# Optimization experiments

Hardware: AMD Instinct MI355X
Metric: run time of the kernel (lower is better)

The kernel has to match this reference:

```python
import jax, jax.numpy as jnp
import numpy as np

B, S, HID = 2, 2048, 2048
H, KV, D = 8, 1, 256
BASE = 10000.0


def setup_inputs() -> dict:
    key = jax.random.key(0)
    ks = jax.random.split(key, 6)
    hidden_states = jax.random.normal(ks[0], (B, S, HID), dtype=jnp.float32)
    attention_mask = jnp.zeros((B, 1, S, S), dtype=jnp.float32)
    position_ids = jnp.sort(jax.random.randint(ks[1], (B, S), 0, S), axis=-1).astype(jnp.int64)
    sc = 1.0 / np.sqrt(HID)
    wq = jax.random.normal(ks[2], (H * D, HID), dtype=jnp.float32) * sc
    wk = jax.random.normal(ks[3], (KV * D, HID), dtype=jnp.float32) * sc
    wv = jax.random.normal(ks[4], (KV * D, HID), dtype=jnp.float32) * sc
    wo = jax.random.normal(ks[5], (HID, H * D), dtype=jnp.float32) * sc
    return {"hidden_states": hidden_states, "attention_mask": attention_mask,
            "position_ids": position_ids, "wq": wq, "wk": wk, "wv": wv, "wo": wo}


def _rotate_half(x):
    x1, x2 = jnp.split(x, 2, axis=-1)
    return jnp.concatenate((-x2, x1), axis=-1)


def reference(hidden_states, attention_mask, position_ids, wq, wk, wv, wo):
    b, s, _ = hidden_states.shape
    # QKV projections (no bias)
    q = (hidden_states @ wq.T).reshape(b, s, H, D).transpose(0, 2, 1, 3)   # [B,H,S,D]
    k = (hidden_states @ wk.T).reshape(b, s, KV, D).transpose(0, 2, 1, 3)  # [B,KV,S,D]
    v = (hidden_states @ wv.T).reshape(b, s, KV, D).transpose(0, 2, 1, 3)
    # RoPE: freqs = pos * inv_freq, emb = cat(freqs, freqs)
    inv_freq = 1.0 / (BASE ** (jnp.arange(0, D, 2, dtype=jnp.float32) / D))  # [D/2]
    freqs = position_ids.astype(jnp.float32)[:, :, None] * inv_freq[None, None, :]  # [B,S,D/2]
    emb = jnp.concatenate((freqs, freqs), axis=-1)                         # [B,S,D]
    cos = jnp.cos(emb)[:, None, :, :].astype(hidden_states.dtype)          # [B,1,S,D]
    sin = jnp.sin(emb)[:, None, :, :].astype(hidden_states.dtype)
    q = q * cos + _rotate_half(q) * sin
    k = k * cos + _rotate_half(k) * sin
    # repeat_kv: kv head outer, rep inner -> jnp.repeat along head axis
    n_rep = H // KV
    k = jnp.repeat(k, n_rep, axis=1)  # [B,H,S,D]
    v = jnp.repeat(v, n_rep, axis=1)
    scores = jnp.einsum('bhqd,bhkd->bhqk', q, k) / jnp.sqrt(jnp.float32(D))
    scores = scores + attention_mask
    attn = jax.nn.softmax(scores.astype(jnp.float32), axis=-1).astype(q.dtype)
    out = jnp.einsum('bhqk,bhkd->bhqd', attn, v)          # [B,H,S,D]
    out = out.transpose(0, 2, 1, 3).reshape(b, s, H * D)  # [B,S,H*D]
    return out @ wo.T
```

## Files before the change

### kernel.cpp

```cpp
#include <hip/hip_runtime.h>
#include <math.h>

#define B_ 2
#define S_ 2048
#define HID_ 2048
#define H_ 8
#define D_ 256
#define KV_STRIDE 512

typedef __attribute__((ext_vector_type(8))) __bf16 bf16x8;
typedef __attribute__((ext_vector_type(8))) unsigned short u16x8;
typedef __attribute__((ext_vector_type(4))) float f32x4;

__device__ __forceinline__ unsigned short bf16_rne(float x) {
    unsigned int u = __float_as_uint(x);
    return (unsigned short)((u + 0x7FFFu + ((u >> 16) & 1u)) >> 16);
}

__global__ __launch_bounds__(256) void split_bf16(const float* __restrict__ x,
                                                  unsigned short* __restrict__ h,
                                                  unsigned short* __restrict__ l,
                                                  int n4) {
    int i = blockIdx.x * 256 + threadIdx.x;
    if (i >= n4) return;
    float4 v = ((const float4*)x)[i];
    ushort4 hh, ll;
    hh.x = bf16_rne(v.x); ll.x = bf16_rne(v.x - __uint_as_float((unsigned int)hh.x << 16));
    hh.y = bf16_rne(v.y); ll.y = bf16_rne(v.y - __uint_as_float((unsigned int)hh.y << 16));
    hh.z = bf16_rne(v.z); ll.z = bf16_rne(v.z - __uint_as_float((unsigned int)hh.z << 16));
    hh.w = bf16_rne(v.w); ll.w = bf16_rne(v.w - __uint_as_float((unsigned int)hh.w << 16));
    ((ushort4*)h)[i] = hh;
    ((ushort4*)l)[i] = ll;
}

__global__ __launch_bounds__(256) void gemm_mfma_split(
    const unsigned short* __restrict__ Ah, const unsigned short* __restrict__ Al,
    const unsigned short* __restrict__ Wh, const unsigned short* __restrict__ Wl,
    float* __restrict__ C, int M, int N, int K)
{
    __shared__ unsigned short As[2][128][40];
    __shared__ unsigned short Bs[2][128][40];

    const int tid  = threadIdx.x;
    const int lane = tid & 63;
    const int w    = tid >> 6;
    const int wr   = w >> 1, wc = w & 1;
    const int fr   = lane & 15;
    const int ko   = (lane >> 4) * 8;
    const int bm   = blockIdx.x * 128, bn = blockIdx.y * 128;

    const int srow = tid >> 1;
    const int skc  = (tid & 1) * 16;
    const unsigned short* gAh = Ah + (size_t)(bm + srow) * K + skc;
    const unsigned short* gAl = Al + (size_t)(bm + srow) * K + skc;
    const unsigned short* gWh = Wh + (size_t)(bn + srow) * K + skc;
    const unsigned short* gWl = Wl + (size_t)(bn + srow) * K + skc;

    f32x4 acc[4][4];
#pragma unroll
    for (int i = 0; i < 4; ++i)
#pragma unroll
        for (int j = 0; j < 4; ++j)
#pragma unroll
            for (int r = 0; r < 4; ++r) acc[i][j][r] = 0.f;

    u16x8 ra0 = ((const u16x8*)gAh)[0], ra1 = ((const u16x8*)gAh)[1];
    u16x8 ra2 = ((const u16x8*)gAl)[0], ra3 = ((const u16x8*)gAl)[1];
    u16x8 rb0 = ((const u16x8*)gWh)[0], rb1 = ((const u16x8*)gWh)[1];
    u16x8 rb2 = ((const u16x8*)gWl)[0], rb3 = ((const u16x8*)gWl)[1];

    for (int k0 = 0; k0 < K; k0 += 32) {
        *(u16x8*)&As[0][srow][skc]     = ra0;
        *(u16x8*)&As[0][srow][skc + 8] = ra1;
        *(u16x8*)&As[1][srow][skc]     = ra2;
        *(u16x8*)&As[1][srow][skc + 8] = ra3;
        *(u16x8*)&Bs[0][srow][skc]     = rb0;
        *(u16x8*)&Bs[0][srow][skc + 8] = rb1;
        *(u16x8*)&Bs[1][srow][skc]     = rb2;
        *(u16x8*)&Bs[1][srow][skc + 8] = rb3;
        __syncthreads();

        if (k0 + 32 < K) {
            const unsigned short* nAh = gAh + k0 + 32;
            const unsigned short* nAl = gAl + k0 + 32;
            const unsigned short* nWh = gWh + k0 + 32;
            const unsigned short* nWl = gWl + k0 + 32;
            ra0 = ((const u16x8*)nAh)[0]; ra1 = ((const u16x8*)nAh)[1];
            ra2 = ((const u16x8*)nAl)[0]; ra3 = ((const u16x8*)nAl)[1];
            rb0 = ((const u16x8*)nWh)[0]; rb1 = ((const u16x8*)nWh)[1];
            rb2 = ((const u16x8*)nWl)[0]; rb3 = ((const u16x8*)nWl)[1];
        }

        bf16x8 ah[4], al4[4], bh[4], bl[4];
#pragma unroll
        for (int i = 0; i < 4; ++i) {
            ah[i]  = *(const bf16x8*)&As[0][wr * 64 + i * 16 + fr][ko];
            al4[i] = *(const bf16x8*)&As[1][wr * 64 + i * 16 + fr][ko];
            bh[i]  = *(const bf16x8*)&Bs[0][wc * 64 + i * 16 + fr][ko];
            bl[i]  = *(const bf16x8*)&Bs[1][wc * 64 + i * 16 + fr][ko];
        }
#pragma unroll
        for (int i = 0; i < 4; ++i)
#pragma unroll
            for (int j = 0; j < 4; ++j) {
                acc[i][j] = __builtin_amdgcn_mfma_f32_16x16x32_bf16(ah[i],  bh[j], acc[i][j], 0, 0, 0);
                acc[i][j] = __builtin_amdgcn_mfma_f32_16x16x32_bf16(ah[i],  bl[j], acc[i][j], 0, 0, 0);
                acc[i][j] = __builtin_amdgcn_mfma_f32_16x16x32_bf16(al4[i], bh[j], acc[i][j], 0, 0, 0);
            }
        __syncthreads();
    }

#pragma unroll
    for (int i = 0; i < 4; ++i) {
        int r0 = bm + wr * 64 + i * 16 + (lane >> 4) * 4;
#pragma unroll
        for (int j = 0; j < 4; ++j) {
            int c = bn + wc * 64 + j * 16 + fr;
#pragma unroll
            for (int r = 0; r < 4; ++r)
                C[(size_t)(r0 + r) * N + c] = acc[i][j][r];
        }
    }
}

__global__ __launch_bounds__(128) void rope_kernel(float* __restrict__ q,
                                                   const float* __restrict__ kv,
                                                   unsigned short* __restrict__ k_h,
                                                   unsigned short* __restrict__ k_l,
                                                   const int* __restrict__ pos) {
    int bs = blockIdx.x;
    int d = threadIdx.x;
    float p = (float)pos[bs];
    float inv = expf(-(2.0f * (float)d / (float)D_) * 9.210340371976184f);
    float sn, cs;
    sincosf(p * inv, &sn, &cs);

    float* qp = q + (size_t)bs * (H_ * D_);
#pragma unroll
    for (int h = 0; h < H_; ++h) {
        float x1 = qp[h * D_ + d];
        float x2 = qp[h * D_ + d + 128];
        qp[h * D_ + d]       = x1 * cs - x2 * sn;
        qp[h * D_ + d + 128] = x2 * cs + x1 * sn;
    }
    const float* kp = kv + (size_t)bs * KV_STRIDE;
    float x1 = kp[d], x2 = kp[d + 128];
    float y1 = x1 * cs - x2 * sn;
    float y2 = x2 * cs + x1 * sn;
    unsigned short h1 = bf16_rne(y1);
    unsigned short h2 = bf16_rne(y2);
    size_t o = (size_t)bs * D_ + d;
    k_h[o]       = h1;
    k_l[o]       = bf16_rne(y1 - __uint_as_float((unsigned int)h1 << 16));
    k_h[o + 128] = h2;
    k_l[o + 128] = bf16_rne(y2 - __uint_as_float((unsigned int)h2 << 16));
}

__global__ __launch_bounds__(256) void vsplitT(const float* __restrict__ kvb,
                                               unsigned short* __restrict__ vTh,
                                               unsigned short* __restrict__ vTl) {
    __shared__ float ts[64][65];
    const int blk = blockIdx.x;
    const int b  = blk >> 7;
    const int dt = (blk >> 5) & 3;
    const int jt = blk & 31;
    const int tid = threadIdx.x;
    const int jj = tid >> 2;
    const int dc = (tid & 3) * 16;
    const float* src = kvb + (size_t)(b * S_ + jt * 64 + jj) * KV_STRIDE + 256 + dt * 64 + dc;
#pragma unroll
    for (int i = 0; i < 16; i += 4) {
        float4 v4 = *(const float4*)(src + i);
        ts[jj][dc + i + 0] = v4.x;
        ts[jj][dc + i + 1] = v4.y;
        ts[jj][dc + i + 2] = v4.z;
        ts[jj][dc + i + 3] = v4.w;
    }
    __syncthreads();
    const int dd = tid >> 2;
    const int jc = (tid & 3) * 16;
    size_t o = (size_t)(b * 256 + dt * 64 + dd) * S_ + jt * 64 + jc;
#pragma unroll
    for (int i = 0; i < 16; i += 8) {
        u16x8 hh, ll;
#pragma unroll
        for (int e = 0; e < 8; ++e) {
            float f = ts[jc + i + e][dd];
            unsigned short hb = bf16_rne(f);
            hh[e] = hb;
            ll[e] = bf16_rne(f - __uint_as_float((unsigned int)hb << 16));
        }
        *(u16x8*)(vTh + o + i) = hh;
        *(u16x8*)(vTl + o + i) = ll;
    }
}

__global__ __launch_bounds__(512) void attn_mfma(
    const float* __restrict__ q,
    const unsigned short* __restrict__ k_h,
    const unsigned short* __restrict__ k_l,
    const unsigned short* __restrict__ vTh,
    const unsigned short* __restrict__ vTl,
    const float* __restrict__ mask,
    float* __restrict__ out)
{
    __shared__ __align__(16) unsigned short Ks[2][16][264];
    __shared__ __align__(16) unsigned short Vs[2][257][24];
    __shared__ __align__(16) unsigned short Ps[2][8][16][40];

    const int tid  = threadIdx.x;
    const int lane = tid & 63;
    const int w    = tid >> 6;
    const int fr   = lane & 15;
    const int kg   = lane >> 4;
    const int nqt  = S_ / 128;
    const int b    = blockIdx.x / (H_ * nqt);
    const int rem  = blockIdx.x % (H_ * nqt);
    const int h    = rem / nqt;
    const int i0   = (rem % nqt) * 128;

    {
        u16x8 z = {0, 0, 0, 0, 0, 0, 0, 0};
        unsigned short* vz = &Vs[0][0][0];
        for (int i = tid * 8; i < 12336; i += 512 * 8)
            *(u16x8*)(vz + i) = z;
        int pp = tid >> 8, pw = (tid >> 5) & 7, pr = (tid >> 1) & 15, ph8 = (tid & 1) * 8;
        *(u16x8*)&Ps[pp][pw][pr][16 + ph8] = z;
    }

    bf16x8 qh[8], ql[8];
    {
        const int qrow = i0 + w * 16 + fr;
        const float* qp = q + (size_t)(b * S_ + qrow) * (H_ * D_) + h * D_ + kg * 8;
#pragma unroll
        for (int ks = 0; ks < 8; ++ks) {
            float4 f0 = *(const float4*)(qp + ks * 32);
            float4 f1 = *(const float4*)(qp + ks * 32 + 4);
            float f[8] = {f0.x, f0.y, f0.z, f0.w, f1.x, f1.y, f1.z, f1.w};
            u16x8 hh, ll;
#pragma unroll
            for (int e = 0; e < 8; ++e) {
                unsigned short hb = bf16_rne(f[e]);
                hh[e] = hb;
                ll[e] = bf16_rne(f[e] - __uint_as_float((unsigned int)hb << 16));
            }
            qh[ks] = *(bf16x8*)&hh;
            ql[ks] = *(bf16x8*)&ll;
        }
    }

    f32x4 acc[16];
#pragma unroll
    for (int cf = 0; cf < 16; ++cf) acc[cf] = f32x4{0.f, 0.f, 0.f, 0.f};
    float m_run[4], l_run[4];
#pragma unroll
    for (int r = 0; r < 4; ++r) { m_run[r] = -1e30f; l_run[r] = 0.f; }

    const int skp = tid >> 8;
    const int skr = (tid >> 4) & 15;
    const int skc = (tid & 15) * 16;
    const int svd = tid & 255;
    const unsigned short* gK = (skp ? k_l : k_h) + (size_t)(b * S_ + skr) * 256 + skc;
    const unsigned short* gV = (skp ? vTl : vTh) + (size_t)(b * 256 + svd) * S_;

    u16x8 rk0 = *(const u16x8*)(gK);
    u16x8 rk1 = *(const u16x8*)(gK + 8);
    u16x8 rv0 = *(const u16x8*)(gV);
    u16x8 rv1 = *(const u16x8*)(gV + 8);

    const float scale = 0.0625f;

    for (int j0 = 0; j0 < S_; j0 += 16) {
        __syncthreads();
        *(u16x8*)&Ks[skp][skr][skc]     = rk0;
        *(u16x8*)&Ks[skp][skr][skc + 8] = rk1;
        *(u16x8*)&Vs[skp][svd][0]       = rv0;
        *(u16x8*)&Vs[skp][svd][8]       = rv1;
        if (j0 + 16 < S_) {
            rk0 = *(const u16x8*)(gK + (size_t)(j0 + 16) * 256);
            rk1 = *(const u16x8*)(gK + (size_t)(j0 + 16) * 256 + 8);
            rv0 = *(const u16x8*)(gV + j0 + 16);
            rv1 = *(const u16x8*)(gV + j0 + 24);
        }
        __syncthreads();

        f32x4 sc = {0.f, 0.f, 0.f, 0.f};
#pragma unroll
        for (int ks = 0; ks < 8; ++ks) {
            bf16x8 bh = *(const bf16x8*)&Ks[0][fr][ks * 32 + kg * 8];
            bf16x8 bl = *(const bf16x8*)&Ks[1][fr][ks * 32 + kg * 8];
            sc = __builtin_amdgcn_mfma_f32_16x16x32_bf16(qh[ks], bh, sc, 0, 0, 0);
            sc = __builtin_amdgcn_mfma_f32_16x16x32_bf16(qh[ks], bl, sc, 0, 0, 0);
            sc = __builtin_amdgcn_mfma_f32_16x16x32_bf16(ql[ks], bh, sc, 0, 0, 0);
        }

        float sv[4];
#pragma unroll
        for (int r = 0; r < 4; ++r)
            sv[r] = sc[r] * scale
                  + mask[(size_t)(b * S_ + i0 + w * 16 + kg * 4 + r) * S_ + j0 + fr];

        float rmax[4];
#pragma unroll
        for (int r = 0; r < 4; ++r) rmax[r] = sv[r];
#pragma unroll
        for (int off = 1; off < 16; off <<= 1)
#pragma unroll
            for (int r = 0; r < 4; ++r)
                rmax[r] = fmaxf(rmax[r], __shfl_xor(rmax[r], off));

        float corr[4], psum[4];
#pragma unroll
        for (int r = 0; r < 4; ++r) {
            float mn = fmaxf(m_run[r], rmax[r]);
            corr[r] = __expf(m_run[r] - mn);
            m_run[r] = mn;
            float p = __expf(sv[r] - mn);
            psum[r] = p;
            unsigned short phh = bf16_rne(p);
            Ps[0][w][kg * 4 + r][fr] = phh;
            Ps[1][w][kg * 4 + r][fr] = bf16_rne(p - __uint_as_float((unsigned int)phh << 16));
        }
#pragma unroll
        for (int off = 1; off < 16; off <<= 1)
#pragma unroll
            for (int r = 0; r < 4; ++r) psum[r] += __shfl_xor(psum[r], off);
#pragma unroll
        for (int r = 0; r < 4; ++r) l_run[r] = l_run[r] * corr[r] + psum[r];

#pragma unroll
        for (int cf = 0; cf < 16; ++cf)
#pragma unroll
            for (int r = 0; r < 4; ++r) acc[cf][r] *= corr[r];

        bf16x8 pah = *(const bf16x8*)&Ps[0][w][fr][kg * 8];
        bf16x8 pal = *(const bf16x8*)&Ps[1][w][fr][kg * 8];
#pragma unroll
        for (int cf = 0; cf < 16; ++cf) {
            bf16x8 vh = *(const bf16x8*)&Vs[0][cf * 16 + fr][kg * 8];
            bf16x8 vl = *(const bf16x8*)&Vs[1][cf * 16 + fr][kg * 8];
            acc[cf] = __builtin_amdgcn_mfma_f32_16x16x32_bf16(pah, vh, acc[cf], 0, 0, 0);
            acc[cf] = __builtin_amdgcn_mfma_f32_16x16x32_bf16(pah, vl, acc[cf], 0, 0, 0);
            acc[cf] = __builtin_amdgcn_mfma_f32_16x16x32_bf16(pal, vh, acc[cf], 0, 0, 0);
        }
    }

#pragma unroll
    for (int r = 0; r < 4; ++r) {
        float invl = 1.0f / l_run[r];
        size_t o = (size_t)(b * S_ + i0 + w * 16 + kg * 4 + r) * (H_ * D_) + h * D_ + fr;
#pragma unroll
        for (int cf = 0; cf < 16; ++cf)
            out[o + cf * 16] = acc[cf][r] * invl;
    }
}

extern "C" void kernel_launch(void* const* d_in, const int* in_sizes, int n_in,
                              void* d_out, int out_size, void* d_ws, size_t ws_size,
                              hipStream_t stream) {
    const float* hs   = (const float*)d_in[0];
    const float* mask = (const float*)d_in[1];
    const int*   pos  = (const int*)d_in[2];
    const float* wq   = (const float*)d_in[3];
    const float* wk   = (const float*)d_in[4];
    const float* wv   = (const float*)d_in[5];
    const float* wo   = (const float*)d_in[6];
    float* out = (float*)d_out;

    char* ws = (char*)d_ws;
    float*          q     = (float*)(ws + 0);
    float*          kvb   = (float*)(ws + 33554432);
    unsigned short* k_h   = (unsigned short*)(ws + 41943040);
    unsigned short* k_l   = (unsigned short*)(ws + 44040192);
    unsigned short* hs_h  = (unsigned short*)(ws + 46137344);
    unsigned short* hs_l  = (unsigned short*)(ws + 62914560);
    float*          ao    = (float*)(ws + 46137344);
    unsigned short* wq_h  = (unsigned short*)(ws + 79691776);
    unsigned short* wq_l  = (unsigned short*)(ws + 88080384);
    unsigned short* vT_h  = (unsigned short*)(ws + 79691776);
    unsigned short* vT_l  = (unsigned short*)(ws + 81788928);
    unsigned short* wkv_h = (unsigned short*)(ws + 96468992);
    unsigned short* wkv_l = (unsigned short*)(ws + 98566144);
    unsigned short* wo_h  = (unsigned short*)(ws + 100663296);
    unsigned short* wo_l  = (unsigned short*)(ws + 109051904);
    unsigned short* ao_h  = (unsigned short*)(ws + 0);
    unsigned short* ao_l  = (unsigned short*)(ws + 16777216);

    const int M = B_ * S_;

    split_bf16<<<dim3(2097152 / 256), dim3(256), 0, stream>>>(hs, hs_h, hs_l, 2097152);
    split_bf16<<<dim3(1048576 / 256), dim3(256), 0, stream>>>(wq, wq_h, wq_l, 1048576);
    split_bf16<<<dim3(131072 / 256),  dim3(256), 0, stream>>>(wk, wkv_h, wkv_l, 131072);
    split_bf16<<<dim3(131072 / 256),  dim3(256), 0, stream>>>(wv, wkv_h + 524288, wkv_l + 524288, 131072);
    split_bf16<<<dim3(1048576 / 256), dim3(256), 0, stream>>>(wo, wo_h, wo_l, 1048576);

    gemm_mfma_split<<<dim3(M / 128, 16), dim3(256), 0, stream>>>(hs_h, hs_l, wq_h, wq_l, q,   M, H_ * D_, HID_);
    gemm_mfma_split<<<dim3(M / 128, 4),  dim3(256), 0, stream>>>(hs_h, hs_l, wkv_h, wkv_l, kvb, M, KV_STRIDE, HID_);

    rope_kernel<<<dim3(B_ * S_), dim3(128), 0, stream>>>(q, kvb, k_h, k_l, pos);
    vsplitT<<<dim3(256), dim3(256), 0, stream>>>(kvb, vT_h, vT_l);

    attn_mfma<<<dim3(B_ * H_ * (S_ / 128)), dim3(512), 0, stream>>>(q, k_h, k_l, vT_h, vT_l, mask, ao);

    split_bf16<<<dim3(2097152 / 256), dim3(256), 0, stream>>>(ao, ao_h, ao_l, 2097152);
    gemm_mfma_split<<<dim3(M / 128, 16), dim3(256), 0, stream>>>(ao_h, ao_l, wo_h, wo_l, out, M, HID_, HID_);
}
```

Measured before the change: 823.8 us.

## Widen attention key tile to 32, restructure LDS layouts, fuse output bf16 split

The attention kernel now processes 32 keys per iteration instead of 16. K, V and P use new shared-memory layouts that hold 8-element vectors, and V is staged in two halves of the head dimension to keep LDS small. The epilogue writes the hi/lo bf16 split of the attention output directly, which removes a separate split kernel and its fp32 round trip through global memory. This halves the number of loop iterations and the barriers per key, but adds two extra barriers per iteration for the second V half, and the new layouts may introduce LDS bank conflicts.

Measured after the change: 722.6 us. 12.3% less time.

```diff
diff --git a/kernel.cpp b/kernel.cpp
--- a/kernel.cpp
+++ b/kernel.cpp
@@ -202,11 +202,12 @@
     const unsigned short* __restrict__ vTh,
     const unsigned short* __restrict__ vTl,
     const float* __restrict__ mask,
-    float* __restrict__ out)
+    unsigned short* __restrict__ aoh,
+    unsigned short* __restrict__ aol)
 {
-    __shared__ __align__(16) unsigned short Ks[2][16][264];
-    __shared__ __align__(16) unsigned short Vs[2][257][24];
-    __shared__ __align__(16) unsigned short Ps[2][8][16][40];
+    __shared__ __align__(16) unsigned short Ks[2][32][32][8];
+    __shared__ __align__(16) unsigned short Vs[2][4][128][8];
+    __shared__ __align__(16) unsigned short Ps[2][8][4][16][8];
 
     const int tid  = threadIdx.x;
     const int lane = tid & 63;
@@ -219,15 +220,6 @@
     const int h    = rem / nqt;
     const int i0   = (rem % nqt) * 128;
 
-    {
-        u16x8 z = {0, 0, 0, 0, 0, 0, 0, 0};
-        unsigned short* vz = &Vs[0][0][0];
-        for (int i = tid * 8; i < 12336; i += 512 * 8)
-            *(u16x8*)(vz + i) = z;
-        int pp = tid >> 8, pw = (tid >> 5) & 7, pr = (tid >> 1) & 15, ph8 = (tid & 1) * 8;
-        *(u16x8*)&Ps[pp][pw][pr][16 + ph8] = z;
-    }
-
     bf16x8 qh[8], ql[8];
     {
         const int qrow = i0 + w * 16 + fr;
@@ -256,53 +248,66 @@
 #pragma unroll
     for (int r = 0; r < 4; ++r) { m_run[r] = -1e30f; l_run[r] = 0.f; }
 
-    const int skp = tid >> 8;
-    const int skr = (tid >> 4) & 15;
-    const int skc = (tid & 15) * 16;
-    const int svd = tid & 255;
-    const unsigned short* gK = (skp ? k_l : k_h) + (size_t)(b * S_ + skr) * 256 + skc;
-    const unsigned short* gV = (skp ? vTl : vTh) + (size_t)(b * 256 + svd) * S_;
-
-    u16x8 rk0 = *(const u16x8*)(gK);
-    u16x8 rk1 = *(const u16x8*)(gK + 8);
-    u16x8 rv0 = *(const u16x8*)(gV);
-    u16x8 rv1 = *(const u16x8*)(gV + 8);
+    const int sp  = tid >> 8;
+    const int t8  = tid & 255;
+    const int sj  = t8 >> 3;
+    const int sdc = (t8 & 7) * 4;
+    const int svd = t8 >> 1;
+    const int sjc = (t8 & 1) * 2;
+    const unsigned short* gK  = (sp ? k_l : k_h) + (size_t)(b * S_ + sj) * 256 + sdc * 8;
+    const unsigned short* gVA = (sp ? vTl : vTh) + (size_t)(b * 256 + svd) * S_ + sjc * 8;
+    const unsigned short* gVB = gVA + (size_t)128 * S_;
+
+    u16x8 rk[4], rva[2], rvb[2];
+#pragma unroll
+    for (int i = 0; i < 4; ++i) rk[i] = *(const u16x8*)(gK + i * 8);
+#pragma unroll
+    for (int i = 0; i < 2; ++i) { rva[i] = *(const u16x8*)(gVA + i * 8);
+                                  rvb[i] = *(const u16x8*)(gVB + i * 8); }
 
     const float scale = 0.0625f;
 
-    for (int j0 = 0; j0 < S_; j0 += 16) {
-        __syncthreads();
-        *(u16x8*)&Ks[skp][skr][skc]     = rk0;
-        *(u16x8*)&Ks[skp][skr][skc + 8] = rk1;
-        *(u16x8*)&Vs[skp][svd][0]       = rv0;
-        *(u16x8*)&Vs[skp][svd][8]       = rv1;
-        if (j0 + 16 < S_) {
-            rk0 = *(const u16x8*)(gK + (size_t)(j0 + 16) * 256);
-            rk1 = *(const u16x8*)(gK + (size_t)(j0 + 16) * 256 + 8);
-            rv0 = *(const u16x8*)(gV + j0 + 16);
-            rv1 = *(const u16x8*)(gV + j0 + 24);
-        }
-        __syncthreads();
-
-        f32x4 sc = {0.f, 0.f, 0.f, 0.f};
+    for (int j0 = 0; j0 < S_; j0 += 32) {
+        __syncthreads();
+#pragma unroll
+        for (int i = 0; i < 4; ++i) *(u16x8*)&Ks[sp][sdc + i][sj][0] = rk[i];
+#pragma unroll
+        for (int i = 0; i < 2; ++i) *(u16x8*)&Vs[sp][sjc + i][svd][0] = rva[i];
+        __syncthreads();
+        if (j0 + 32 < S_) {
+#pragma unroll
+            for (int i = 0; i < 4; ++i) rk[i]  = *(const u16x8*)(gK  + (size_t)(j0 + 32) * 256 + i * 8);
+#pragma unroll
+            for (int i = 0; i < 2; ++i) rva[i] = *(const u16x8*)(gVA + (j0 + 32) + i * 8);
+        }
+
+        f32x4 sc0 = {0.f, 0.f, 0.f, 0.f}, sc1 = {0.f, 0.f, 0.f, 0.f};
 #pragma unroll
         for (int ks = 0; ks < 8; ++ks) {
-            bf16x8 bh = *(const bf16x8*)&Ks[0][fr][ks * 32 + kg * 8];
-            bf16x8 bl = *(const bf16x8*)&Ks[1][fr][ks * 32 + kg * 8];
-            sc = __builtin_amdgcn_mfma_f32_16x16x32_bf16(qh[ks], bh, sc, 0, 0, 0);
-            sc = __builtin_amdgcn_mfma_f32_16x16x32_bf16(qh[ks], bl, sc, 0, 0, 0);
-            sc = __builtin_amdgcn_mfma_f32_16x16x32_bf16(ql[ks], bh, sc, 0, 0, 0);
-        }
-
-        float sv[4];
-#pragma unroll
-        for (int r = 0; r < 4; ++r)
-            sv[r] = sc[r] * scale
-                  + mask[(size_t)(b * S_ + i0 + w * 16 + kg * 4 + r) * S_ + j0 + fr];
+            const int dc = ks * 4 + kg;
+            bf16x8 bh0 = *(const bf16x8*)&Ks[0][dc][fr][0];
+            bf16x8 bl0 = *(const bf16x8*)&Ks[1][dc][fr][0];
+            bf16x8 bh1 = *(const bf16x8*)&Ks[0][dc][16 + fr][0];
+            bf16x8 bl1 = *(const bf16x8*)&Ks[1][dc][16 + fr][0];
+            sc0 = __builtin_amdgcn_mfma_f32_16x16x32_bf16(qh[ks], bh0, sc0, 0, 0, 0);
+            sc0 = __builtin_amdgcn_mfma_f32_16x16x32_bf16(qh[ks], bl0, sc0, 0, 0, 0);
+            sc0 = __builtin_amdgcn_mfma_f32_16x16x32_bf16(ql[ks], bh0, sc0, 0, 0, 0);
+            sc1 = __builtin_amdgcn_mfma_f32_16x16x32_bf16(qh[ks], bh1, sc1, 0, 0, 0);
+            sc1 = __builtin_amdgcn_mfma_f32_16x16x32_bf16(qh[ks], bl1, sc1, 0, 0, 0);
+            sc1 = __builtin_amdgcn_mfma_f32_16x16x32_bf16(ql[ks], bh1, sc1, 0, 0, 0);
+        }
+
+        float sv0[4], sv1[4];
+        const float* mrow = &mask[(size_t)(b * S_ + i0 + w * 16 + kg * 4) * S_ + j0 + fr];
+#pragma unroll
+        for (int r = 0; r < 4; ++r) {
+            sv0[r] = sc0[r] * scale + mrow[(size_t)r * S_];
+            sv1[r] = sc1[r] * scale + mrow[(size_t)r * S_ + 16];
+        }
 
         float rmax[4];
 #pragma unroll
-        for (int r = 0; r < 4; ++r) rmax[r] = sv[r];
+        for (int r = 0; r < 4; ++r) rmax[r] = fmaxf(sv0[r], sv1[r]);
 #pragma unroll
         for (int off = 1; off < 16; off <<= 1)
 #pragma unroll
@@ -315,11 +320,15 @@
             float mn = fmaxf(m_run[r], rmax[r]);
             corr[r] = __expf(m_run[r] - mn);
             m_run[r] = mn;
-            float p = __expf(sv[r] - mn);
-            psum[r] = p;
-            unsigned short phh = bf16_rne(p);
-            Ps[0][w][kg * 4 + r][fr] = phh;
-            Ps[1][w][kg * 4 + r][fr] = bf16_rne(p - __uint_as_float((unsigned int)phh << 16));
+            float p0 = __expf(sv0[r] - mn);
+            float p1 = __expf(sv1[r] - mn);
+            psum[r] = p0 + p1;
+            unsigned short p0h = bf16_rne(p0);
+            unsigned short p1h = bf16_rne(p1);
+            Ps[0][w][(fr >> 3)][kg * 4 + r][fr & 7]     = p0h;
+            Ps[1][w][(fr >> 3)][kg * 4 + r][fr & 7]     = bf16_rne(p0 - __uint_as_float((unsigned int)p0h << 16));
+            Ps[0][w][2 + (fr >> 3)][kg * 4 + r][fr & 7] = p1h;
+            Ps[1][w][2 + (fr >> 3)][kg * 4 + r][fr & 7] = bf16_rne(p1 - __uint_as_float((unsigned int)p1h << 16));
         }
 #pragma unroll
         for (int off = 1; off < 16; off <<= 1)
@@ -328,21 +337,39 @@
 #pragma unroll
         for (int r = 0; r < 4; ++r) l_run[r] = l_run[r] * corr[r] + psum[r];
 
+        bf16x8 pah = *(const bf16x8*)&Ps[0][w][kg][fr][0];
+        bf16x8 pal = *(const bf16x8*)&Ps[1][w][kg][fr][0];
+
 #pragma unroll
         for (int cf = 0; cf < 16; ++cf)
 #pragma unroll
             for (int r = 0; r < 4; ++r) acc[cf][r] *= corr[r];
 
-        bf16x8 pah = *(const bf16x8*)&Ps[0][w][fr][kg * 8];
-        bf16x8 pal = *(const bf16x8*)&Ps[1][w][fr][kg * 8];
-#pragma unroll
-        for (int cf = 0; cf < 16; ++cf) {
-            bf16x8 vh = *(const bf16x8*)&Vs[0][cf * 16 + fr][kg * 8];
-            bf16x8 vl = *(const bf16x8*)&Vs[1][cf * 16 + fr][kg * 8];
+#pragma unroll
+        for (int cf = 0; cf < 8; ++cf) {
+            bf16x8 vh = *(const bf16x8*)&Vs[0][kg][cf * 16 + fr][0];
+            bf16x8 vl = *(const bf16x8*)&Vs[1][kg][cf * 16 + fr][0];
             acc[cf] = __builtin_amdgcn_mfma_f32_16x16x32_bf16(pah, vh, acc[cf], 0, 0, 0);
             acc[cf] = __builtin_amdgcn_mfma_f32_16x16x32_bf16(pah, vl, acc[cf], 0, 0, 0);
             acc[cf] = __builtin_amdgcn_mfma_f32_16x16x32_bf16(pal, vh, acc[cf], 0, 0, 0);
         }
+
+        __syncthreads();
+#pragma unroll
+        for (int i = 0; i < 2; ++i) *(u16x8*)&Vs[sp][sjc + i][svd][0] = rvb[i];
+        __syncthreads();
+        if (j0 + 32 < S_)
+#pragma unroll
+            for (int i = 0; i < 2; ++i) rvb[i] = *(const u16x8*)(gVB + (j0 + 32) + i * 8);
+
+#pragma unroll
+        for (int cf = 8; cf < 16; ++cf) {
+            bf16x8 vh = *(const bf16x8*)&Vs[0][kg][(cf - 8) * 16 + fr][0];
+            bf16x8 vl = *(const bf16x8*)&Vs[1][kg][(cf - 8) * 16 + fr][0];
+            acc[cf] = __builtin_amdgcn_mfma_f32_16x16x32_bf16(pah, vh, acc[cf], 0, 0, 0);
+            acc[cf] = __builtin_amdgcn_mfma_f32_16x16x32_bf16(pah, vl, acc[cf], 0, 0, 0);
+            acc[cf] = __builtin_amdgcn_mfma_f32_16x16x32_bf16(pal, vh, acc[cf], 0, 0, 0);
+        }
     }
 
 #pragma unroll
@@ -350,8 +377,12 @@
         float invl = 1.0f / l_run[r];
         size_t o = (size_t)(b * S_ + i0 + w * 16 + kg * 4 + r) * (H_ * D_) + h * D_ + fr;
 #pragma unroll
-        for (int cf = 0; cf < 16; ++cf)
-            out[o + cf * 16] = acc[cf][r] * invl;
+        for (int cf = 0; cf < 16; ++cf) {
+            float v = acc[cf][r] * invl;
+            unsigned short hb = bf16_rne(v);
+            aoh[o + cf * 16] = hb;
+            aol[o + cf * 16] = bf16_rne(v - __uint_as_float((unsigned int)hb << 16));
+        }
     }
 }
 
@@ -374,7 +405,8 @@
     unsigned short* k_l   = (unsigned short*)(ws + 44040192);
     unsigned short* hs_h  = (unsigned short*)(ws + 46137344);
     unsigned short* hs_l  = (unsigned short*)(ws + 62914560);
-    float*          ao    = (float*)(ws + 46137344);
+    unsigned short* ao_h  = (unsigned short*)(ws + 46137344);
+    unsigned short* ao_l  = (unsigned short*)(ws + 62914560);
     unsigned short* wq_h  = (unsigned short*)(ws + 79691776);
     unsigned short* wq_l  = (unsigned short*)(ws + 88080384);
     unsigned short* vT_h  = (unsigned short*)(ws + 79691776);
@@ -383,8 +415,6 @@
     unsigned short* wkv_l = (unsigned short*)(ws + 98566144);
     unsigned short* wo_h  = (unsigned short*)(ws + 100663296);
     unsigned short* wo_l  = (unsigned short*)(ws + 109051904);
-    unsigned short* ao_h  = (unsigned short*)(ws + 0);
-    unsigned short* ao_l  = (unsigned short*)(ws + 16777216);
 
     const int M = B_ * S_;
 
@@ -400,8 +430,7 @@
     rope_kernel<<<dim3(B_ * S_), dim3(128), 0, stream>>>(q, kvb, k_h, k_l, pos);
     vsplitT<<<dim3(256), dim3(256), 0, stream>>>(kvb, vT_h, vT_l);
 
-    attn_mfma<<<dim3(B_ * H_ * (S_ / 128)), dim3(512), 0, stream>>>(q, k_h, k_l, vT_h, vT_l, mask, ao);
-
-    split_bf16<<<dim3(2097152 / 256), dim3(256), 0, stream>>>(ao, ao_h, ao_l, 2097152);
+    attn_mfma<<<dim3(B_ * H_ * (S_ / 128)), dim3(512), 0, stream>>>(q, k_h, k_l, vT_h, vT_l, mask, ao_h, ao_l);
+
     gemm_mfma_split<<<dim3(M / 128, 16), dim3(256), 0, stream>>>(ao_h, ao_l, wo_h, wo_l, out, M, HID_, HID_);
 }
```
